# Kernel tuning notes

Hardware: AMD Instinct MI355X
Metric: run time of the kernel (lower is better)

## Reference

```python
import jax, jax.numpy as jnp
import numpy as np

EPS_BN = 1e-5
EPS_SIM = 1e-8
PAD = 1
NUM_ITERS = 3


def capsule_conv2d(x, w):
    # x: [B, C, H, W]; w: [out_caps, in_caps, kh, kw, in_len, out_len]
    B, C, H, W = x.shape
    oc, ic, kh, kw, il, ol = w.shape
    # im2col patches, feature dim ordered (c, kh, kw) -> matches torch.unfold
    patches = jax.lax.conv_general_dilated_patches(
        x, (kh, kw), (1, 1), [(PAD, PAD), (PAD, PAD)])  # [B, C*kh*kw, H, W]
    N = H * W
    p = patches.reshape(B, ic, il, kh * kw, N)
    p = jnp.transpose(p, (0, 4, 1, 3, 2))  # [B, N, ic, kk, il]
    wf = w.reshape(oc, ic, kh * kw, il, ol)
    # per-patch capsule transform -> priors [B, N, oc, ic*kk, ol]
    priors = jnp.einsum('bnikl,oiklm->bnoikm', p, wf)
    priors = priors.reshape(B, N, oc, ic * kh * kw, ol)
    # k-means routing with Tonimoto similarity, 3 iterations, no squash
    out = priors.mean(axis=-2, keepdims=True)  # [B, N, oc, 1, ol]
    for _ in range(NUM_ITERS):
        dot = jnp.sum(priors * out, axis=-1, keepdims=True)
        n1 = jnp.sum(priors * priors, axis=-1, keepdims=True)
        n2 = jnp.sum(out * out, axis=-1, keepdims=True)
        logits = dot / jnp.maximum(n1 + n2 - dot, EPS_SIM)
        probs = jax.nn.softmax(logits, axis=-2)
        out = jnp.sum(probs * priors, axis=-2, keepdims=True)
    out = out[..., 0, :]                      # [B, N, oc, ol]
    out = out.reshape(B, H, W, oc * ol)       # channels = oc*ol
    return jnp.transpose(out, (0, 3, 1, 2))   # [B, C, H, W]


def batchnorm2d(x, gamma, beta):
    mean = x.mean(axis=(0, 2, 3), keepdims=True)
    var = x.var(axis=(0, 2, 3), keepdims=True)  # biased, as torch BN training fwd
    inv = jax.lax.rsqrt(var + EPS_BN)
    return gamma[None, :, None, None] * (x - mean) * inv + beta[None, :, None, None]


def setup_inputs() -> dict:
    key = jax.random.key(0)
    k0, k1, k2 = jax.random.split(key, 3)
    B, C, H, W = 2, 64, 96, 96
    IL = OL = 8
    x = jax.random.normal(k0, (B, C, H, W), jnp.float32)
    w1 = jax.random.normal(k1, (C // OL, C // IL, 3, 3, IL, OL), jnp.float32) * 0.1
    w2 = jax.random.normal(k2, (C // OL, C // OL, 3, 3, OL, OL), jnp.float32) * 0.1
    g1 = jnp.ones((C,), jnp.float32)
    b1 = jnp.zeros((C,), jnp.float32)
    g2 = jnp.ones((C,), jnp.float32)
    b2 = jnp.zeros((C,), jnp.float32)
    return {"x": x, "w1": w1, "g1": g1, "b1": b1, "w2": w2, "g2": g2, "b2": b2}


def reference(x, w1, g1, b1, w2, g2, b2):
    r = batchnorm2d(capsule_conv2d(x, w1), g1, b1)
    r = batchnorm2d(capsule_conv2d(r, w2), g2, b2)
    return x + r
```

## Files before the change

### kernel.cpp

```cpp
#include <hip/hip_runtime.h>
#include <hip/hip_bf16.h>

#define HW 9216
#define NPC 18432
#define NELEM 1179648
#define PSTR 584
#define XSTR 72
#define PATCH_B 7776
#define PRL_O 18688

typedef __attribute__((ext_vector_type(2))) float f32x2;
typedef __attribute__((ext_vector_type(4))) float f32x4v;
typedef __attribute__((ext_vector_type(8))) short short8v;

__device__ __forceinline__ f32x2 fma2(f32x2 a, f32x2 b, f32x2 c) {
#if __has_builtin(__builtin_elementwise_fma)
    return __builtin_elementwise_fma(a, b, c);
#else
    return f32x2{fmaf(a.x, b.x, c.x), fmaf(a.y, b.y, c.y)};
#endif
}
__device__ __forceinline__ float dot8v(f32x2 a0, f32x2 a1, f32x2 a2, f32x2 a3,
                                       f32x2 b0, f32x2 b1, f32x2 b2, f32x2 b3) {
    f32x2 acc = a0 * b0;
    acc = fma2(a1, b1, acc);
    acc = fma2(a2, b2, acc);
    acc = fma2(a3, b3, acc);
    return acc.x + acc.y;
}

template <int CTRL>
__device__ __forceinline__ float dpp_add(float x) {
    int y = __builtin_amdgcn_update_dpp(0, __float_as_int(x), CTRL, 0xF, 0xF, true);
    return x + __int_as_float(y);
}
__device__ __forceinline__ float red_lo(float x) {
    x = dpp_add<0xB1>(x);
    x = dpp_add<0x4E>(x);
    x = dpp_add<0x141>(x);
    return x;
}

__device__ __forceinline__ int detect_is32(const unsigned short* __restrict__ w1u) {
    int lane = threadIdx.x & 63;
    int bad = 0;
    #pragma unroll
    for (int i = 0; i < 16; ++i) {
        unsigned short u = (unsigned short)(w1u[lane + i * 64] & 0x7FFF);
        bad |= (u >= 0x42C8);
    }
    return (__ballot(bad) != 0ULL) ? 1 : 0;
}

__device__ __forceinline__ float load_in(const void* p, int idx, int is32) {
    return is32 ? ((const float*)p)[idx]
                : __bfloat162float(((const __hip_bfloat16*)p)[idx]);
}

__device__ __forceinline__ float lo16(unsigned v) { return __int_as_float((int)(v << 16)); }
__device__ __forceinline__ float hi16(unsigned v) { return __int_as_float((int)(v & 0xFFFF0000u)); }
__device__ __forceinline__ unsigned short bf16b(float f) {
    __hip_bfloat16 h = __float2bfloat16(f);
    return *(unsigned short*)&h;
}

__launch_bounds__(256)
__global__ void prep_kernel(const void* __restrict__ x,
                            const void* __restrict__ w1, const void* __restrict__ w2,
                            float* __restrict__ xt,
                            __hip_bfloat16* __restrict__ Bfr1,
                            __hip_bfloat16* __restrict__ Bfr2,
                            float* __restrict__ statz) {
    __shared__ float tile[64 * 33];
    const int bid = blockIdx.x;
    if (bid < 576) {
        const int is32 = detect_is32((const unsigned short*)w1);
        int xb = bid % 3, y = (bid / 3) % 96, b = bid / 288;
        int x0 = xb * 32;
        for (int e = threadIdx.x; e < 2048; e += 256) {
            int xl = e & 31, c = e >> 5;
            tile[c * 33 + xl] = load_in(x, ((b * 64 + c) * 96 + y) * 96 + x0 + xl, is32);
        }
        __syncthreads();
        for (int f = threadIdx.x; f < 2048; f += 256) {
            int c = f & 63, xl = f >> 6;
            xt[((b * 96 + y) * 96 + x0 + xl) * 64 + c] = tile[c * 33 + xl];
        }
    } else if (bid < 720) {
        const int is32 = detect_is32((const unsigned short*)w1);
        int t = (bid - 576) * 256 + threadIdx.x;
        int layer = t / 18432;
        int r = t - layer * 18432;
        int lane = r & 63;
        int fi = r >> 6;
        int h = fi & 1, g = (fi >> 1) & 1;
        int kq = fi >> 2;
        int k = kq % 9, o = kq / 9;
        int dy = k / 3, dx = k % 3;
        int quad = lane >> 4, colhi = (lane >> 3) & 1, m = lane & 7;
        int act = (quad == 2 * h + colhi);
        int i = g * 4 + 2 * h + colhi;
        const void* w = layer ? w2 : w1;
        __hip_bfloat16* dst = layer ? Bfr2 : Bfr1;
        #pragma unroll
        for (int j = 0; j < 8; ++j) {
            float v = act ? load_in(w, ((((o * 8 + i) * 3 + dy) * 3 + dx) * 8 + j) * 8 + m, is32)
                          : 0.f;
            dst[(fi * 64 + lane) * 8 + j] = __float2bfloat16(v);
        }
    } else {
        for (int e = threadIdx.x; e < 2048; e += 256) statz[e] = 0.f;
    }
}

__launch_bounds__(256, 3)
__global__ void caps_kernel(const float* __restrict__ in,
                            const float* __restrict__ statPrev,
                            const void* __restrict__ gamma, const void* __restrict__ beta,
                            const void* __restrict__ wdt,
                            const __hip_bfloat16* __restrict__ Bfr,
                            float* __restrict__ yout,
                            float* __restrict__ statL,
                            int layer1) {
    __shared__ __align__(16) unsigned char smem[PATCH_B + 2 * PRL_O];
    __hip_bfloat16* patchH = (__hip_bfloat16*)smem;
    __hip_bfloat16* prH    = (__hip_bfloat16*)(smem + PATCH_B);
    float* omF = (float*)smem;
    float* scL = (float*)(smem + PATCH_B);
    float* shL = scL + 64;

    const int gx    = blockIdx.x;
    const int opair = gx & 3;
    const int x0    = (gx >> 2) * 16;
    const int y  = blockIdx.y;
    const int b  = blockIdx.z;
    const int tid = threadIdx.x;

    if (!layer1) {
        if (tid < 64) {
            const int is32 = detect_is32((const unsigned short*)wdt);
            int c = tid;
            float s = 0.f, ss = 0.f;
            #pragma unroll
            for (int cp = 0; cp < 8; ++cp) {
                s  += statPrev[cp * 128 + c];
                ss += statPrev[cp * 128 + 64 + c];
            }
            float mean = s * (1.f / (float)NPC);
            float var  = fmaxf(ss * (1.f / (float)NPC) - mean * mean, 0.f);
            float inv  = rsqrtf(var + 1e-5f);
            float g = load_in(gamma, c, is32) * inv;
            scL[c] = g;
            shL[c] = load_in(beta, c, is32) - mean * g;
        }
        __syncthreads();
    }

    for (int e = tid; e < 1728; e += 256) {
        int c2 = e & 31;
        int q  = e >> 5;
        int xo = q % 18, row = q / 18;
        int yy = y + row - 1, xx = x0 + xo - 1;
        float va = 0.f, vb = 0.f;
        if (yy >= 0 && yy < 96 && xx >= 0 && xx < 96) {
            const float* p = &in[((b * 96 + yy) * 96 + xx) * 64 + c2 * 2];
            va = p[0]; vb = p[1];
            if (!layer1) {
                va = va * scL[c2 * 2]     + shL[c2 * 2];
                vb = vb * scL[c2 * 2 + 1] + shL[c2 * 2 + 1];
            }
        }
        unsigned pk = ((unsigned)bf16b(vb) << 16) | (unsigned)bf16b(va);
        *(unsigned*)&patchH[q * XSTR + c2 * 2] = pk;
    }
    __syncthreads();

    const int lane = tid & 63;
    const int wv   = tid >> 6;
    const int o2w  = wv >> 1;
    const int g    = wv & 1;

    {
        const int o     = opair * 2 + o2w;
        const int rowA  = lane & 15;
        const int quad  = lane >> 4;
        const int colhi = (lane >> 3) & 1;
        const int m     = lane & 7;
        __hip_bfloat16* prBase = prH + o2w * (PRL_O / 2) * 1;
        #pragma unroll
        for (int k = 0; k < 9; ++k) {
            const int dy = k / 3, dx = k % 3;
            short8v a = *(const short8v*)&patchH[(dy * 18 + dx + rowA) * XSTR + g * 32 + quad * 8];
            #pragma unroll
            for (int h = 0; h < 2; ++h) {
                short8v bf = *(const short8v*)&Bfr[((((o * 9 + k) * 2 + g) * 2 + h) * 64 + lane) * 8];
                f32x4v d = __builtin_amdgcn_mfma_f32_16x16x32_bf16(a, bf, (f32x4v){0.f, 0.f, 0.f, 0.f}, 0, 0, 0);
                const int iw = g * 4 + 2 * h + colhi;
                const int basei = (iw * 9 + k) * 8 + m;
                #pragma unroll
                for (int r = 0; r < 4; ++r)
                    prBase[(quad * 4 + r) * PSTR + basei] = __float2bfloat16(d[r]);
            }
        }
    }
    __syncthreads();

    const int unit = tid >> 3;
    const int o2   = unit >> 4;
    const int pos  = unit & 15;
    const int i    = tid & 7;
    const __hip_bfloat16* pb = &prH[o2 * (PRL_O / 2) + pos * PSTR + i * 72];

    uint4 u[9];
    #pragma unroll
    for (int k = 0; k < 9; ++k) u[k] = *(const uint4*)(pb + k * 8);

    f32x2 fr[36];
    float n1[9];
    #pragma unroll
    for (int k = 0; k < 9; ++k) {
        fr[4 * k + 0] = f32x2{lo16(u[k].x), hi16(u[k].x)};
        fr[4 * k + 1] = f32x2{lo16(u[k].y), hi16(u[k].y)};
        fr[4 * k + 2] = f32x2{lo16(u[k].z), hi16(u[k].z)};
        fr[4 * k + 3] = f32x2{lo16(u[k].w), hi16(u[k].w)};
    }

    f32x2 om2[4];
    {
        f32x2 s2[4] = {f32x2{0.f, 0.f}, f32x2{0.f, 0.f}, f32x2{0.f, 0.f}, f32x2{0.f, 0.f}};
        #pragma unroll
        for (int k = 0; k < 9; ++k) {
            s2[0] += fr[4 * k + 0];
            s2[1] += fr[4 * k + 1];
            s2[2] += fr[4 * k + 2];
            s2[3] += fr[4 * k + 3];
        }
        #pragma unroll
        for (int q = 0; q < 4; ++q) {
            om2[q].x = red_lo(s2[q].x) * (1.f / 72.f);
            om2[q].y = red_lo(s2[q].y) * (1.f / 72.f);
        }
    }
    float n2 = dot8v(om2[0], om2[1], om2[2], om2[3], om2[0], om2[1], om2[2], om2[3]);

    #pragma unroll
    for (int it = 0; it < 3; ++it) {
        float se = 0.f;
        f32x2 acc2[4] = {f32x2{0.f, 0.f}, f32x2{0.f, 0.f}, f32x2{0.f, 0.f}, f32x2{0.f, 0.f}};
        #pragma unroll
        for (int k = 0; k < 9; ++k) {
            if (it == 0)
                n1[k] = dot8v(fr[4 * k], fr[4 * k + 1], fr[4 * k + 2], fr[4 * k + 3],
                              fr[4 * k], fr[4 * k + 1], fr[4 * k + 2], fr[4 * k + 3]);
            float d = dot8v(fr[4 * k], fr[4 * k + 1], fr[4 * k + 2], fr[4 * k + 3],
                            om2[0], om2[1], om2[2], om2[3]);
            float denom = fmaxf(n1[k] + n2 - d, 1e-8f);
            float e = __expf(d * __builtin_amdgcn_rcpf(denom));
            se += e;
            f32x2 ev{e, e};
            acc2[0] = fma2(ev, fr[4 * k + 0], acc2[0]);
            acc2[1] = fma2(ev, fr[4 * k + 1], acc2[1]);
            acc2[2] = fma2(ev, fr[4 * k + 2], acc2[2]);
            acc2[3] = fma2(ev, fr[4 * k + 3], acc2[3]);
        }
        se = red_lo(se);
        #pragma unroll
        for (int q = 0; q < 4; ++q) {
            acc2[q].x = red_lo(acc2[q].x);
            acc2[q].y = red_lo(acc2[q].y);
        }
        float inv = __builtin_amdgcn_rcpf(se);
        f32x2 iv{inv, inv};
        #pragma unroll
        for (int q = 0; q < 4; ++q) om2[q] = acc2[q] * iv;
        n2 = dot8v(om2[0], om2[1], om2[2], om2[3], om2[0], om2[1], om2[2], om2[3]);
    }

    if (i == 0) {
        const int o = opair * 2 + o2;
        float4 o0 = {om2[0].x, om2[0].y, om2[1].x, om2[1].y};
        float4 o1 = {om2[2].x, om2[2].y, om2[3].x, om2[3].y};
        float* dst = &yout[((b * 96 + y) * 96 + x0 + pos) * 64 + o * 8];
        *(float4*)dst = o0;
        *(float4*)(dst + 4) = o1;
        *(float4*)&omF[unit * 8] = o0;
        *(float4*)&omF[unit * 8 + 4] = o1;
    }
    __syncthreads();

    if (tid < 32) {
        int c16 = tid & 15, sel = tid >> 4;
        int oo2 = c16 >> 3, m = c16 & 7;
        float v = 0.f;
        #pragma unroll
        for (int pp = 0; pp < 16; ++pp) {
            float t = omF[(oo2 * 16 + pp) * 8 + m];
            v += sel ? t * t : t;
        }
        int cp = (blockIdx.x + blockIdx.y * 3 + blockIdx.z) & 7;
        atomicAdd(&statL[cp * 128 + sel * 64 + (opair * 2 + oo2) * 8 + m], v);
    }
}

__launch_bounds__(256)
__global__ void final_kernel(const void* __restrict__ xin,
                             const float* __restrict__ yt2,
                             const float* __restrict__ statL,
                             const void* __restrict__ gamma, const void* __restrict__ beta,
                             const void* __restrict__ w1,
                             void* __restrict__ outp) {
    __shared__ float tile[64 * 33];
    __shared__ float scL[64], shL[64];
    const int is32 = detect_is32((const unsigned short*)w1);
    if (threadIdx.x < 64) {
        int c = threadIdx.x;
        float s = 0.f, ss = 0.f;
        #pragma unroll
        for (int cp = 0; cp < 8; ++cp) {
            s  += statL[cp * 128 + c];
            ss += statL[cp * 128 + 64 + c];
        }
        float mean = s * (1.f / (float)NPC);
        float var  = fmaxf(ss * (1.f / (float)NPC) - mean * mean, 0.f);
        float inv  = rsqrtf(var + 1e-5f);
        float g = load_in(gamma, c, is32) * inv;
        scL[c] = g;
        shL[c] = load_in(beta, c, is32) - mean * g;
    }
    __syncthreads();

    int x0 = blockIdx.x * 32, y = blockIdx.y, b = blockIdx.z;
    for (int e = threadIdx.x; e < 2048; e += 256) {
        int c = e & 63, xl = e >> 6;
        float v = yt2[((b * 96 + y) * 96 + x0 + xl) * 64 + c];
        tile[c * 33 + xl] = v * scL[c] + shL[c];
    }
    __syncthreads();
    for (int f = threadIdx.x; f < 2048; f += 256) {
        int xl = f & 31, c = f >> 5;
        int idx = ((b * 64 + c) * 96 + y) * 96 + x0 + xl;
        float v = load_in(xin, idx, is32) + tile[c * 33 + xl];
        if (is32) ((float*)outp)[idx] = v;
        else      ((__hip_bfloat16*)outp)[idx] = __float2bfloat16(v);
    }
}

extern "C" void kernel_launch(void* const* d_in, const int* in_sizes, int n_in,
                              void* d_out, int out_size, void* d_ws, size_t ws_size,
                              hipStream_t stream) {
    const void* x  = d_in[0];
    const void* w1 = d_in[1];
    const void* g1 = d_in[2];
    const void* b1 = d_in[3];
    const void* w2 = d_in[4];
    const void* g2 = d_in[5];
    const void* b2 = d_in[6];

    float* ws   = (float*)d_ws;
    float* bufA = ws;
    float* bufB = bufA + NELEM;
    __hip_bfloat16* Bfr1 = (__hip_bfloat16*)(bufB + NELEM);
    __hip_bfloat16* Bfr2 = Bfr1 + 147456;
    float* statz = (float*)(Bfr2 + 147456);
    float* statL1 = statz;
    float* statL2 = statz + 1024;

    prep_kernel<<<721, 256, 0, stream>>>(x, w1, w2, bufA, Bfr1, Bfr2, statz);

    dim3 cgrid(24, 96, 2);
    caps_kernel<<<cgrid, 256, 0, stream>>>(bufA, nullptr, nullptr, nullptr, w1,
                                           Bfr1, bufB, statL1, 1);
    caps_kernel<<<cgrid, 256, 0, stream>>>(bufB, statL1, g1, b1, w1,
                                           Bfr2, bufA, statL2, 0);
    final_kernel<<<dim3(3, 96, 2), 256, 0, stream>>>(x, bufA, statL2, g2, b2, w1, d_out);
}
```

Before: 191.8 us.

## Store intermediate activations in bf16 and pack prior stores via DPP

Intermediate NHWC activation buffers (prep output, layer outputs) become bf16 instead of fp32, which halves global traffic for the patch gathers and the final kernel. The patch loads widen to uint2 per thread. Prior stores from the MFMA results pair adjacent lanes with a DPP swap, so each even lane writes a packed 32-bit value instead of two 16-bit writes. Rounding the layer outputs to bf16 before BN adds precision loss, though the caps kernel already rounded these values to bf16 on load.

New measurement: 232.0 us. 20.9% more time.

```diff
diff --git a/kernel.cpp b/kernel.cpp
--- a/kernel.cpp
+++ b/kernel.cpp
@@ -59,15 +59,15 @@
 
 __device__ __forceinline__ float lo16(unsigned v) { return __int_as_float((int)(v << 16)); }
 __device__ __forceinline__ float hi16(unsigned v) { return __int_as_float((int)(v & 0xFFFF0000u)); }
-__device__ __forceinline__ unsigned short bf16b(float f) {
-    __hip_bfloat16 h = __float2bfloat16(f);
-    return *(unsigned short*)&h;
+__device__ __forceinline__ unsigned pk2bf(float a, float b) {
+    __hip_bfloat162 h = __float22bfloat162_rn(float2{a, b});
+    return *(unsigned*)&h;
 }
 
 __launch_bounds__(256)
 __global__ void prep_kernel(const void* __restrict__ x,
                             const void* __restrict__ w1, const void* __restrict__ w2,
-                            float* __restrict__ xt,
+                            __hip_bfloat16* __restrict__ xt,
                             __hip_bfloat16* __restrict__ Bfr1,
                             __hip_bfloat16* __restrict__ Bfr2,
                             float* __restrict__ statz) {
@@ -82,9 +82,11 @@
             tile[c * 33 + xl] = load_in(x, ((b * 64 + c) * 96 + y) * 96 + x0 + xl, is32);
         }
         __syncthreads();
-        for (int f = threadIdx.x; f < 2048; f += 256) {
-            int c = f & 63, xl = f >> 6;
-            xt[((b * 96 + y) * 96 + x0 + xl) * 64 + c] = tile[c * 33 + xl];
+        for (int f = threadIdx.x; f < 1024; f += 256) {
+            int c2 = f & 31, xl = f >> 5;
+            float a = tile[(2 * c2) * 33 + xl];
+            float c = tile[(2 * c2 + 1) * 33 + xl];
+            *(unsigned*)&xt[((b * 96 + y) * 96 + x0 + xl) * 64 + 2 * c2] = pk2bf(a, c);
         }
     } else if (bid < 720) {
         const int is32 = detect_is32((const unsigned short*)w1);
@@ -114,12 +116,12 @@
 }
 
 __launch_bounds__(256, 3)
-__global__ void caps_kernel(const float* __restrict__ in,
+__global__ void caps_kernel(const __hip_bfloat16* __restrict__ in,
                             const float* __restrict__ statPrev,
                             const void* __restrict__ gamma, const void* __restrict__ beta,
                             const void* __restrict__ wdt,
                             const __hip_bfloat16* __restrict__ Bfr,
-                            float* __restrict__ yout,
+                            __hip_bfloat16* __restrict__ yout,
                             float* __restrict__ statL,
                             int layer1) {
     __shared__ __align__(16) unsigned char smem[PATCH_B + 2 * PRL_O];
@@ -156,22 +158,25 @@
         __syncthreads();
     }
 
-    for (int e = tid; e < 1728; e += 256) {
-        int c2 = e & 31;
-        int q  = e >> 5;
+    for (int e = tid; e < 864; e += 256) {
+        int c4 = e & 15;
+        int q  = e >> 4;
         int xo = q % 18, row = q / 18;
         int yy = y + row - 1, xx = x0 + xo - 1;
-        float va = 0.f, vb = 0.f;
+        uint2 v = {0u, 0u};
         if (yy >= 0 && yy < 96 && xx >= 0 && xx < 96) {
-            const float* p = &in[((b * 96 + yy) * 96 + xx) * 64 + c2 * 2];
-            va = p[0]; vb = p[1];
+            v = *(const uint2*)&in[((b * 96 + yy) * 96 + xx) * 64 + c4 * 4];
             if (!layer1) {
-                va = va * scL[c2 * 2]     + shL[c2 * 2];
-                vb = vb * scL[c2 * 2 + 1] + shL[c2 * 2 + 1];
+                int c = c4 * 4;
+                float f0 = lo16(v.x) * scL[c]     + shL[c];
+                float f1 = hi16(v.x) * scL[c + 1] + shL[c + 1];
+                float f2 = lo16(v.y) * scL[c + 2] + shL[c + 2];
+                float f3 = hi16(v.y) * scL[c + 3] + shL[c + 3];
+                v.x = pk2bf(f0, f1);
+                v.y = pk2bf(f2, f3);
             }
         }
-        unsigned pk = ((unsigned)bf16b(vb) << 16) | (unsigned)bf16b(va);
-        *(unsigned*)&patchH[q * XSTR + c2 * 2] = pk;
+        *(uint2*)&patchH[q * XSTR + c4 * 4] = v;
     }
     __syncthreads();
 
@@ -186,7 +191,7 @@
         const int quad  = lane >> 4;
         const int colhi = (lane >> 3) & 1;
         const int m     = lane & 7;
-        __hip_bfloat16* prBase = prH + o2w * (PRL_O / 2) * 1;
+        __hip_bfloat16* prBase = prH + o2w * 9344;
         #pragma unroll
         for (int k = 0; k < 9; ++k) {
             const int dy = k / 3, dx = k % 3;
@@ -198,8 +203,12 @@
                 const int iw = g * 4 + 2 * h + colhi;
                 const int basei = (iw * 9 + k) * 8 + m;
                 #pragma unroll
-                for (int r = 0; r < 4; ++r)
-                    prBase[(quad * 4 + r) * PSTR + basei] = __float2bfloat16(d[r]);
+                for (int r = 0; r < 4; ++r) {
+                    int prt = __builtin_amdgcn_update_dpp(0, __float_as_int(d[r]), 0xB1, 0xF, 0xF, true);
+                    unsigned pk = pk2bf(d[r], __int_as_float(prt));
+                    if ((m & 1) == 0)
+                        *(unsigned*)&prBase[(quad * 4 + r) * PSTR + basei] = pk;
+                }
             }
         }
     }
@@ -209,7 +218,7 @@
     const int o2   = unit >> 4;
     const int pos  = unit & 15;
     const int i    = tid & 7;
-    const __hip_bfloat16* pb = &prH[o2 * (PRL_O / 2) + pos * PSTR + i * 72];
+    const __hip_bfloat16* pb = &prH[o2 * 9344 + pos * PSTR + i * 72];
 
     uint4 u[9];
     #pragma unroll
@@ -278,11 +287,14 @@
 
     if (i == 0) {
         const int o = opair * 2 + o2;
+        uint4 pk;
+        pk.x = pk2bf(om2[0].x, om2[0].y);
+        pk.y = pk2bf(om2[1].x, om2[1].y);
+        pk.z = pk2bf(om2[2].x, om2[2].y);
+        pk.w = pk2bf(om2[3].x, om2[3].y);
+        *(uint4*)&yout[((b * 96 + y) * 96 + x0 + pos) * 64 + o * 8] = pk;
         float4 o0 = {om2[0].x, om2[0].y, om2[1].x, om2[1].y};
         float4 o1 = {om2[2].x, om2[2].y, om2[3].x, om2[3].y};
-        float* dst = &yout[((b * 96 + y) * 96 + x0 + pos) * 64 + o * 8];
-        *(float4*)dst = o0;
-        *(float4*)(dst + 4) = o1;
         *(float4*)&omF[unit * 8] = o0;
         *(float4*)&omF[unit * 8 + 4] = o1;
     }
@@ -304,7 +316,7 @@
 
 __launch_bounds__(256)
 __global__ void final_kernel(const void* __restrict__ xin,
-                             const float* __restrict__ yt2,
+                             const __hip_bfloat16* __restrict__ yt2,
                              const float* __restrict__ statL,
                              const void* __restrict__ gamma, const void* __restrict__ beta,
                              const void* __restrict__ w1,
@@ -330,10 +342,12 @@
     __syncthreads();
 
     int x0 = blockIdx.x * 32, y = blockIdx.y, b = blockIdx.z;
-    for (int e = threadIdx.x; e < 2048; e += 256) {
-        int c = e & 63, xl = e >> 6;
-        float v = yt2[((b * 96 + y) * 96 + x0 + xl) * 64 + c];
-        tile[c * 33 + xl] = v * scL[c] + shL[c];
+    for (int e = threadIdx.x; e < 1024; e += 256) {
+        int c2 = e & 31, xl = e >> 5;
+        unsigned v = *(const unsigned*)&yt2[((b * 96 + y) * 96 + x0 + xl) * 64 + c2 * 2];
+        int c = c2 * 2;
+        tile[c * 33 + xl]       = lo16(v) * scL[c]     + shL[c];
+        tile[(c + 1) * 33 + xl] = hi16(v) * scL[c + 1] + shL[c + 1];
     }
     __syncthreads();
     for (int f = threadIdx.x; f < 2048; f += 256) {
@@ -356,10 +370,9 @@
     const void* g2 = d_in[5];
     const void* b2 = d_in[6];
 
-    float* ws   = (float*)d_ws;
-    float* bufA = ws;
-    float* bufB = bufA + NELEM;
-    __hip_bfloat16* Bfr1 = (__hip_bfloat16*)(bufB + NELEM);
+    __hip_bfloat16* bufA = (__hip_bfloat16*)d_ws;
+    __hip_bfloat16* bufB = bufA + NELEM;
+    __hip_bfloat16* Bfr1 = bufB + NELEM;
     __hip_bfloat16* Bfr2 = Bfr1 + 147456;
     float* statz = (float*)(Bfr2 + 147456);
     float* statL1 = statz;
```
